# Performance work log

Hardware: AMD Instinct MI355X
Metric: run time of the kernel (lower is better)

## Reference

```python
import jax, jax.numpy as jnp
import numpy as np

N_WINDOWS = 4
WIN_H, WIN_W = 512, 512          # module 'size'
IMG_H, IMG_W = 1024, 1024        # 2x2 tiling of windows
N_MASKS = 32                     # n_windows * masks_per_window
MPW = N_MASKS // N_WINDOWS       # 8 masks per window (channel 0 of each block = background)
SLOT_DIM = 64
SIM_THRESH = 0.1                 # module 'similarity'


def setup_inputs() -> dict:
    key = jax.random.key(0)
    k1, k2 = jax.random.split(key)
    masks = jax.random.normal(k1, (1, N_MASKS, IMG_H, IMG_W), dtype=jnp.float32)
    slot_features = jax.random.normal(k2, (N_WINDOWS, MPW - 1, SLOT_DIM), dtype=jnp.float32)
    # static window layout, equivalent to keys ['w_0_0','w_512_0','w_0_512','w_512_512']
    pad_left = jnp.array([0, WIN_W, 0, WIN_W], dtype=jnp.int32)
    pad_top = jnp.array([0, 0, WIN_H, WIN_H], dtype=jnp.int32)
    return {"masks": masks, "slot_features": slot_features,
            "pad_left": pad_left, "pad_top": pad_top}


def _merge_windows(masks, slot_features, pl, pt):
    """pl, pt: python int lists (static metadata parsed from keys)."""
    B, C, H, W = masks.shape
    mpw = C // N_WINDOWS

    # --- to_one_hot: argmax over channel dim, one-hot back to [B,C,H,W] float ---
    ids = jnp.argmax(masks, axis=1)                                   # [B,H,W]
    m = jnp.moveaxis(jax.nn.one_hot(ids, C, dtype=masks.dtype), -1, 1)  # [B,C,H,W]

    ranges = [(i * mpw, (i + 1) * mpw) for i in range(N_WINDOWS)]

    # --- adjacency over window pads (static) ---
    adjacency = []
    for i in range(N_WINDOWS):
        for j in range(i + 1, N_WINDOWS):
            if pt[i] == pt[j] and abs(pl[i] - pl[j]) == WIN_W:
                adjacency.append((i, j, True) if pl[i] < pl[j] else (j, i, True))
            if pl[i] == pl[j] and abs(pt[i] - pt[j]) == WIN_H:
                adjacency.append((i, j, False) if pt[i] < pt[j] else (j, i, False))

    # --- per-channel edge-touch booleans (vectorized replacement of set building) ---
    edge_l = jnp.zeros((C,), bool)
    edge_r = jnp.zeros((C,), bool)
    edge_t = jnp.zeros((C,), bool)
    edge_b = jnp.zeros((C,), bool)
    for wi, (s, e) in enumerate(ranges):
        ys, ye = max(pt[wi], 0), min(pt[wi] + WIN_H, H)
        xs, xe = max(pl[wi], 0), min(pl[wi] + WIN_W, W)
        if ys >= ye or xs >= xe:
            continue
        win = m[0, s:e, ys:ye, xs:xe]                # [mpw, hh, ww]
        edge_l = edge_l.at[s:e].set(jnp.any(win[:, :, 0] == 1, axis=-1))
        edge_r = edge_r.at[s:e].set(jnp.any(win[:, :, -1] == 1, axis=-1))
        edge_t = edge_t.at[s:e].set(jnp.any(win[:, 0, :] == 1, axis=-1))
        edge_b = edge_b.at[s:e].set(jnp.any(win[:, -1, :] == 1, axis=-1))

    # --- static candidate pair list (background channels ci % mpw == 0 excluded) ---
    ci_l, cj_l, wi_l, wj_l, hz_l = [], [], [], [], []
    for wi, wj, horiz in adjacency:
        si, ei = ranges[wi]
        sj, ej = ranges[wj]
        for ci in range(si + 1, ei):
            for cj in range(sj + 1, ej):
                ci_l.append(ci); cj_l.append(cj)
                wi_l.append(wi); wj_l.append(wj); hz_l.append(horiz)
    P = len(ci_l)
    if P == 0:
        return m

    ci_a = jnp.array(ci_l, jnp.int32)
    cj_a = jnp.array(cj_l, jnp.int32)
    horiz = jnp.array(hz_l)

    # --- cosine similarities for all pairs at once ---
    sf_n = slot_features / (jnp.linalg.norm(slot_features, axis=-1, keepdims=True) + 1e-8)
    rel_i = np.array(ci_l) % mpw - 1
    rel_j = np.array(cj_l) % mpw - 1
    fi = sf_n[np.array(wi_l), rel_i]                 # [P, D]
    fj = sf_n[np.array(wj_l), rel_j]
    sims = jnp.sum(fi * fj, axis=-1)                 # [P]

    edge_ok = jnp.where(horiz, edge_r[ci_a] & edge_l[cj_a], edge_b[ci_a] & edge_t[cj_a])
    passing = edge_ok & (sims > SIM_THRESH)          # [P]

    # --- sequential dedup/merge scan (order-dependent, like the torch loop) ---
    def step(carry, xs):
        m, merged = carry
        ci, cj, ok = xs
        cond = ok & ~merged[ci] & ~merged[cj]
        keep = jnp.minimum(ci, cj)
        rem = jnp.maximum(ci, cj)
        rem_ch = jnp.take(m, rem, axis=1)            # [B,H,W]
        m = m.at[:, keep].add(jnp.where(cond, rem_ch, 0.0))
        m = m.at[:, rem].set(jnp.where(cond, jnp.zeros_like(rem_ch), rem_ch))
        merged = merged.at[rem].set(merged[rem] | cond)
        return (m, merged), None

    (m, _), _ = jax.lax.scan(step, (m, jnp.zeros((C,), bool)), (ci_a, cj_a, passing))
    return m


def reference(masks, slot_features, pad_left, pad_top):
    # pads encode the (static) window layout parsed from the string keys
    pl = [int(v) for v in np.asarray(pad_left)]
    pt = [int(v) for v in np.asarray(pad_top)]
    return _merge_windows(masks, slot_features, pl, pt)
```

## Files before the change

### kernel.cpp

```cpp
#include <hip/hip_runtime.h>

#define IMG_H 1024
#define IMG_W 1024
#define NPIX (IMG_H * IMG_W)
#define N_MASKS 32
#define N_WINDOWS 4
#define MPW 8
#define WIN_H 512
#define WIN_W 512
#define SIM_THRESH 0.1f
#define NBLK 1024

typedef float vf4 __attribute__((ext_vector_type(4)));

#define WS_EDGE  0
#define WS_IDS   (NBLK * 16)

__global__ __launch_bounds__(256) void k_argmax(const float* __restrict__ masks,
                                                const int* __restrict__ pl,
                                                const int* __restrict__ pt,
                                                uint4* __restrict__ edge_blocks,
                                                unsigned char* __restrict__ ids) {
    __shared__ int spl[4], spt[4];
    __shared__ unsigned sem[4];
    const int tid = threadIdx.x;
    if (tid < 4) { spl[tid] = pl[tid]; spt[tid] = pt[tid]; sem[tid] = 0u; }
    __syncthreads();

    const int idx = (blockIdx.x * 256 + tid) * 4;

    float bv0, bv1, bv2, bv3;
    int bc0 = 0, bc1 = 0, bc2 = 0, bc3 = 0;
    {
        const float4 v = *(const float4*)(masks + idx);
        bv0 = v.x; bv1 = v.y; bv2 = v.z; bv3 = v.w;
    }
#pragma unroll
    for (int c = 1; c < N_MASKS; c++) {
        const float4 v = *(const float4*)(masks + (size_t)c * NPIX + idx);
        if (v.x > bv0) { bv0 = v.x; bc0 = c; }
        if (v.y > bv1) { bv1 = v.y; bc1 = c; }
        if (v.z > bv2) { bv2 = v.z; bc2 = c; }
        if (v.w > bv3) { bv3 = v.w; bc3 = c; }
    }
    *(uchar4*)(ids + idx) = make_uchar4((unsigned char)bc0, (unsigned char)bc1,
                                        (unsigned char)bc2, (unsigned char)bc3);

    const int y = idx >> 10;
    const int x0 = idx & (IMG_W - 1);
    const int bcs[4] = {bc0, bc1, bc2, bc3};
#pragma unroll
    for (int wi = 0; wi < N_WINDOWS; wi++) {
        const int xs = max(spl[wi], 0), xe = min(spl[wi] + WIN_W, IMG_W);
        const int ys = max(spt[wi], 0), ye = min(spt[wi] + WIN_H, IMG_H);
        if (ys >= ye || xs >= xe) continue;
        if (y < ys || y >= ye) continue;
#pragma unroll
        for (int k = 0; k < 4; k++) {
            const int x = x0 + k;
            if (x < xs || x >= xe) continue;
            const int c = bcs[k];
            if ((c >> 3) != wi) continue;
            const unsigned bit = 1u << c;
            if (x == xs)     atomicOr(&sem[0], bit);
            if (x == xe - 1) atomicOr(&sem[1], bit);
            if (y == ys)     atomicOr(&sem[2], bit);
            if (y == ye - 1) atomicOr(&sem[3], bit);
        }
    }
    __syncthreads();
    if (tid == 0) edge_blocks[blockIdx.x] = make_uint4(sem[0], sem[1], sem[2], sem[3]);
}

__global__ __launch_bounds__(256) void k_merge_write(const unsigned char* __restrict__ ids,
                                                     const float* __restrict__ sf,
                                                     const int* __restrict__ pl,
                                                     const int* __restrict__ pt,
                                                     const uint4* __restrict__ edge_blocks,
                                                     float* __restrict__ out) {
    __shared__ float sfn[28 * 65];
    __shared__ unsigned step_word[512];
    __shared__ uint4 wred[4];
    __shared__ unsigned fedge[4];
    __shared__ int sP;
    __shared__ int loc[32];

    const int tid = threadIdx.x;
    const int lane = tid & 63;
    const int wave = tid >> 6;

    unsigned el = 0, er = 0, et = 0, eb = 0;
    for (int b = tid; b < NBLK; b += 256) {
        const uint4 w = edge_blocks[b];
        el |= w.x; er |= w.y; et |= w.z; eb |= w.w;
    }
#pragma unroll
    for (int off = 1; off < 64; off <<= 1) {
        el |= __shfl_xor(el, off);
        er |= __shfl_xor(er, off);
        et |= __shfl_xor(et, off);
        eb |= __shfl_xor(eb, off);
    }
    if (lane == 0) wred[wave] = make_uint4(el, er, et, eb);

#pragma unroll
    for (int i = 0; i < 7; i++) {
        const int r = wave + 4 * i;
        const float v = sf[r * 64 + lane];
        float s = v * v;
#pragma unroll
        for (int off = 1; off < 64; off <<= 1) s += __shfl_xor(s, off);
        sfn[r * 65 + lane] = v * (1.0f / (sqrtf(s) + 1e-8f));
    }
    __syncthreads();

    if (tid == 0) {
        unsigned fl = wred[0].x | wred[1].x | wred[2].x | wred[3].x;
        unsigned fr = wred[0].y | wred[1].y | wred[2].y | wred[3].y;
        unsigned ft = wred[0].z | wred[1].z | wred[2].z | wred[3].z;
        unsigned fb = wred[0].w | wred[1].w | wred[2].w | wred[3].w;
        fedge[0] = fl; fedge[1] = fr; fedge[2] = ft; fedge[3] = fb;

        int lpl[4], lpt[4];
        for (int i = 0; i < 4; i++) { lpl[i] = pl[i]; lpt[i] = pt[i]; }
        int aI[8], aJ[8], aH[8], na = 0;
        for (int i = 0; i < N_WINDOWS; i++)
            for (int j = i + 1; j < N_WINDOWS; j++) {
                if (lpt[i] == lpt[j] && abs(lpl[i] - lpl[j]) == WIN_W) {
                    if (lpl[i] < lpl[j]) { aI[na] = i; aJ[na] = j; }
                    else                 { aI[na] = j; aJ[na] = i; }
                    aH[na] = 1; na++;
                }
                if (lpl[i] == lpl[j] && abs(lpt[i] - lpt[j]) == WIN_H) {
                    if (lpt[i] < lpt[j]) { aI[na] = i; aJ[na] = j; }
                    else                 { aI[na] = j; aJ[na] = i; }
                    aH[na] = 0; na++;
                }
            }
        int P = 0;
        for (int a = 0; a < na; a++)
            for (int ci = aI[a] * MPW + 1; ci < (aI[a] + 1) * MPW; ci++)
                for (int cj = aJ[a] * MPW + 1; cj < (aJ[a] + 1) * MPW; cj++)
                    step_word[P++] = (unsigned)ci | ((unsigned)cj << 8)
                                   | ((unsigned)aH[a] << 16);
        sP = P;
    }
    __syncthreads();

    const int P = sP;
    {
        const unsigned ger = fedge[1], gel = fedge[0], geb = fedge[3], get = fedge[2];
        for (int p = tid; p < P; p += 256) {
            const unsigned w = step_word[p];
            const int ci = w & 255, cj = (w >> 8) & 255, hz = (w >> 16) & 1;
            const float* fi = &sfn[((ci >> 3) * (MPW - 1) + (ci & 7) - 1) * 65];
            const float* fj = &sfn[((cj >> 3) * (MPW - 1) + (cj & 7) - 1) * 65];
            float s = 0.f;
#pragma unroll
            for (int k = 0; k < 64; k++) s += fi[k] * fj[k];
            const bool eok = hz ? (((ger >> ci) & 1u) && ((gel >> cj) & 1u))
                                : (((geb >> ci) & 1u) && ((get >> cj) & 1u));
            if (eok && s > SIM_THRESH) step_word[p] = w | (1u << 17);
        }
    }
    __syncthreads();

    if (wave == 0) {
        unsigned merged = 0;
        int myloc = lane;
        for (int p = 0; p < P; p++) {
            const unsigned w = step_word[p];
            if (w >> 17) {
                const int ci = w & 255, cj = (w >> 8) & 255;
                if (!((merged >> ci) & 1u) && !((merged >> cj) & 1u)) {
                    const int keep = min(ci, cj), rem = max(ci, cj);
                    if (myloc == rem) myloc = keep;
                    merged |= 1u << rem;
                }
            }
        }
        if (lane < 32) loc[lane] = myloc;
    }
    __syncthreads();

    const int idx = (blockIdx.x * 256 + tid) * 4;
    const uchar4 id4 = *(const uchar4*)(ids + idx);
    const int r0 = loc[id4.x], r1 = loc[id4.y], r2 = loc[id4.z], r3 = loc[id4.w];
#pragma unroll
    for (int c = 0; c < N_MASKS; c++) {
        vf4 v;
        v.x = (r0 == c) ? 1.0f : 0.0f;
        v.y = (r1 == c) ? 1.0f : 0.0f;
        v.z = (r2 == c) ? 1.0f : 0.0f;
        v.w = (r3 == c) ? 1.0f : 0.0f;
        __builtin_nontemporal_store(v, (vf4*)(out + (size_t)c * NPIX + idx));
    }
}

extern "C" void kernel_launch(void* const* d_in, const int* in_sizes, int n_in,
                              void* d_out, int out_size, void* d_ws, size_t ws_size,
                              hipStream_t stream) {
    const float* masks = (const float*)d_in[0];
    const float* sf    = (const float*)d_in[1];
    const int*   pl    = (const int*)d_in[2];
    const int*   pt    = (const int*)d_in[3];
    float* out = (float*)d_out;

    char* ws = (char*)d_ws;
    uint4* edge_blocks = (uint4*)(ws + WS_EDGE);
    unsigned char* ids = (unsigned char*)(ws + WS_IDS);

    k_argmax<<<NBLK, 256, 0, stream>>>(masks, pl, pt, edge_blocks, ids);
    k_merge_write<<<NBLK, 256, 0, stream>>>(ids, sf, pl, pt, edge_blocks, out);
}
```

Before: 262.2 us.

## Fuse argmax and merge-write into one kernel with inter-block flag sync

Replaces the two kernels with one. Eight blocks recompute argmax only along the window border pixels to build the edge masks, and block 8 builds the merge table from them. All blocks compute their own argmax and spin-wait on a global flag before writing the one-hot output. This removes the per-pixel ids round-trip through memory, the per-block edge atomics and the second launch. In exchange it relies on the low-index blocks being resident, and it never resets the MAGIC flags between calls, so a later call can read stale merge results.

Measured after the change: 578.7 us. +120.7%, slower.

```diff
diff --git a/kernel.cpp b/kernel.cpp
--- a/kernel.cpp
+++ b/kernel.cpp
@@ -10,25 +10,172 @@
 #define WIN_W 512
 #define SIM_THRESH 0.1f
 #define NBLK 1024
+#define MAGIC 0x13579BDFu
 
 typedef float vf4 __attribute__((ext_vector_type(4)));
 
-#define WS_EDGE  0
-#define WS_IDS   (NBLK * 16)
-
-__global__ __launch_bounds__(256) void k_argmax(const float* __restrict__ masks,
-                                                const int* __restrict__ pl,
-                                                const int* __restrict__ pt,
-                                                uint4* __restrict__ edge_blocks,
-                                                unsigned char* __restrict__ ids) {
+
+__global__ __launch_bounds__(256, 4) void k_fused(const float* __restrict__ masks,
+                                                  const float* __restrict__ sf,
+                                                  const int* __restrict__ pl,
+                                                  const int* __restrict__ pt,
+                                                  unsigned* __restrict__ ws,
+                                                  float* __restrict__ out) {
+    unsigned* edges = ws;
+    unsigned* bflag = ws + 32;
+    unsigned* locg  = ws + 48;
+    unsigned* lflag = ws + 80;
+
     __shared__ int spl[4], spt[4];
-    __shared__ unsigned sem[4];
+    __shared__ unsigned segmask[2];
+    __shared__ int sloc[32];
+    __shared__ float sfn[28 * 65];
+    __shared__ unsigned step_word[512];
+    __shared__ unsigned fedge[4];
+    __shared__ int sP;
+
     const int tid = threadIdx.x;
-    if (tid < 4) { spl[tid] = pl[tid]; spt[tid] = pt[tid]; sem[tid] = 0u; }
+    const int lane = tid & 63;
+    const int wave = tid >> 6;
+    const int b = blockIdx.x;
+
+    if (tid < 4) { spl[tid] = pl[tid]; spt[tid] = pt[tid]; }
+    if (tid < 2) segmask[tid] = 0u;
     __syncthreads();
 
-    const int idx = (blockIdx.x * 256 + tid) * 4;
-
+    if (b < 8) {
+        for (int k = 0; k < 2; k++) {
+            const int s = 2 * b + k;
+            const int wi = s >> 2, side = s & 3;
+            const int xs = max(spl[wi], 0), xe = min(spl[wi] + WIN_W, IMG_W);
+            const int ys = max(spt[wi], 0), ye = min(spt[wi] + WIN_H, IMG_H);
+            if (ys >= ye || xs >= xe) continue;
+            const int L = (side < 2) ? (ye - ys) : (xe - xs);
+            for (int u = tid; u < L; u += 256) {
+                int x, y;
+                if      (side == 0) { x = xs;     y = ys + u; }
+                else if (side == 1) { x = xe - 1; y = ys + u; }
+                else if (side == 2) { y = ys;     x = xs + u; }
+                else                { y = ye - 1; x = xs + u; }
+                const int p = y * IMG_W + x;
+                float bv = masks[p];
+                int bc = 0;
+#pragma unroll
+                for (int c = 1; c < N_MASKS; c++) {
+                    const float v = masks[(size_t)c * NPIX + p];
+                    if (v > bv) { bv = v; bc = c; }
+                }
+                if ((bc >> 3) == wi) atomicOr(&segmask[k], 1u << bc);
+            }
+        }
+        __syncthreads();
+        if (tid == 0) {
+            unsigned e[4] = {0u, 0u, 0u, 0u};
+            e[(2 * b) & 3]     |= segmask[0];
+            e[(2 * b + 1) & 3] |= segmask[1];
+#pragma unroll
+            for (int i = 0; i < 4; i++)
+                __hip_atomic_store(&edges[4 * b + i], e[i],
+                                   __ATOMIC_RELAXED, __HIP_MEMORY_SCOPE_AGENT);
+            __hip_atomic_store(&bflag[b], MAGIC,
+                               __ATOMIC_RELEASE, __HIP_MEMORY_SCOPE_AGENT);
+        }
+    } else if (b == 8) {
+        if (tid < 8) {
+            while (__hip_atomic_load(&bflag[tid], __ATOMIC_ACQUIRE,
+                                     __HIP_MEMORY_SCOPE_AGENT) != MAGIC)
+                __builtin_amdgcn_s_sleep(8);
+        }
+        __syncthreads();
+        if (tid == 0) {
+            unsigned e0 = 0, e1 = 0, e2 = 0, e3 = 0;
+            for (int i = 0; i < 8; i++) {
+                e0 |= __hip_atomic_load(&edges[4 * i + 0], __ATOMIC_RELAXED, __HIP_MEMORY_SCOPE_AGENT);
+                e1 |= __hip_atomic_load(&edges[4 * i + 1], __ATOMIC_RELAXED, __HIP_MEMORY_SCOPE_AGENT);
+                e2 |= __hip_atomic_load(&edges[4 * i + 2], __ATOMIC_RELAXED, __HIP_MEMORY_SCOPE_AGENT);
+                e3 |= __hip_atomic_load(&edges[4 * i + 3], __ATOMIC_RELAXED, __HIP_MEMORY_SCOPE_AGENT);
+            }
+            fedge[0] = e0; fedge[1] = e1; fedge[2] = e2; fedge[3] = e3;
+        }
+#pragma unroll
+        for (int i = 0; i < 7; i++) {
+            const int r = wave + 4 * i;
+            const float v = sf[r * 64 + lane];
+            float s2 = v * v;
+#pragma unroll
+            for (int off = 1; off < 64; off <<= 1) s2 += __shfl_xor(s2, off);
+            sfn[r * 65 + lane] = v * (1.0f / (sqrtf(s2) + 1e-8f));
+        }
+        __syncthreads();
+        if (tid == 0) {
+            int lpl[4], lpt[4];
+            for (int i = 0; i < 4; i++) { lpl[i] = spl[i]; lpt[i] = spt[i]; }
+            int aI[8], aJ[8], aH[8], na = 0;
+            for (int i = 0; i < N_WINDOWS; i++)
+                for (int j = i + 1; j < N_WINDOWS; j++) {
+                    if (lpt[i] == lpt[j] && abs(lpl[i] - lpl[j]) == WIN_W) {
+                        if (lpl[i] < lpl[j]) { aI[na] = i; aJ[na] = j; }
+                        else                 { aI[na] = j; aJ[na] = i; }
+                        aH[na] = 1; na++;
+                    }
+                    if (lpl[i] == lpl[j] && abs(lpt[i] - lpt[j]) == WIN_H) {
+                        if (lpt[i] < lpt[j]) { aI[na] = i; aJ[na] = j; }
+                        else                 { aI[na] = j; aJ[na] = i; }
+                        aH[na] = 0; na++;
+                    }
+                }
+            int P = 0;
+            for (int a = 0; a < na; a++)
+                for (int ci = aI[a] * MPW + 1; ci < (aI[a] + 1) * MPW; ci++)
+                    for (int cj = aJ[a] * MPW + 1; cj < (aJ[a] + 1) * MPW; cj++)
+                        step_word[P++] = (unsigned)ci | ((unsigned)cj << 8)
+                                       | ((unsigned)aH[a] << 16);
+            sP = P;
+        }
+        __syncthreads();
+        const int P = sP;
+        {
+            const unsigned gel = fedge[0], ger = fedge[1], get = fedge[2], geb = fedge[3];
+            for (int p = tid; p < P; p += 256) {
+                const unsigned w = step_word[p];
+                const int ci = w & 255, cj = (w >> 8) & 255, hz = (w >> 16) & 1;
+                const float* fi = &sfn[((ci >> 3) * (MPW - 1) + (ci & 7) - 1) * 65];
+                const float* fj = &sfn[((cj >> 3) * (MPW - 1) + (cj & 7) - 1) * 65];
+                float s = 0.f;
+#pragma unroll
+                for (int k2 = 0; k2 < 64; k2++) s += fi[k2] * fj[k2];
+                const bool eok = hz ? (((ger >> ci) & 1u) && ((gel >> cj) & 1u))
+                                    : (((geb >> ci) & 1u) && ((get >> cj) & 1u));
+                if (eok && s > SIM_THRESH) step_word[p] = w | (1u << 17);
+            }
+        }
+        __syncthreads();
+        if (wave == 0) {
+            unsigned merged = 0;
+            int myloc = lane;
+            for (int p = 0; p < P; p++) {
+                const unsigned w = step_word[p];
+                if (w >> 17) {
+                    const int ci = w & 255, cj = (w >> 8) & 255;
+                    if (!((merged >> ci) & 1u) && !((merged >> cj) & 1u)) {
+                        const int keep = min(ci, cj), rem = max(ci, cj);
+                        if (myloc == rem) myloc = keep;
+                        merged |= 1u << rem;
+                    }
+                }
+            }
+            if (lane < 32)
+                __hip_atomic_store(&locg[lane], (unsigned)myloc,
+                                   __ATOMIC_RELAXED, __HIP_MEMORY_SCOPE_AGENT);
+        }
+        __syncthreads();
+        if (tid == 0) {
+            __threadfence();
+            __hip_atomic_store(lflag, MAGIC, __ATOMIC_RELEASE, __HIP_MEMORY_SCOPE_AGENT);
+        }
+    }
+
+    const int idx = (b * 256 + tid) * 4;
     float bv0, bv1, bv2, bv3;
     int bc0 = 0, bc1 = 0, bc2 = 0, bc3 = 0;
     {
@@ -43,149 +190,19 @@
         if (v.z > bv2) { bv2 = v.z; bc2 = c; }
         if (v.w > bv3) { bv3 = v.w; bc3 = c; }
     }
-    *(uchar4*)(ids + idx) = make_uchar4((unsigned char)bc0, (unsigned char)bc1,
-                                        (unsigned char)bc2, (unsigned char)bc3);
-
-    const int y = idx >> 10;
-    const int x0 = idx & (IMG_W - 1);
-    const int bcs[4] = {bc0, bc1, bc2, bc3};
-#pragma unroll
-    for (int wi = 0; wi < N_WINDOWS; wi++) {
-        const int xs = max(spl[wi], 0), xe = min(spl[wi] + WIN_W, IMG_W);
-        const int ys = max(spt[wi], 0), ye = min(spt[wi] + WIN_H, IMG_H);
-        if (ys >= ye || xs >= xe) continue;
-        if (y < ys || y >= ye) continue;
-#pragma unroll
-        for (int k = 0; k < 4; k++) {
-            const int x = x0 + k;
-            if (x < xs || x >= xe) continue;
-            const int c = bcs[k];
-            if ((c >> 3) != wi) continue;
-            const unsigned bit = 1u << c;
-            if (x == xs)     atomicOr(&sem[0], bit);
-            if (x == xe - 1) atomicOr(&sem[1], bit);
-            if (y == ys)     atomicOr(&sem[2], bit);
-            if (y == ye - 1) atomicOr(&sem[3], bit);
-        }
+
+    if (tid == 0) {
+        while (__hip_atomic_load(lflag, __ATOMIC_ACQUIRE,
+                                 __HIP_MEMORY_SCOPE_AGENT) != MAGIC)
+            __builtin_amdgcn_s_sleep(8);
     }
     __syncthreads();
-    if (tid == 0) edge_blocks[blockIdx.x] = make_uint4(sem[0], sem[1], sem[2], sem[3]);
-}
-
-__global__ __launch_bounds__(256) void k_merge_write(const unsigned char* __restrict__ ids,
-                                                     const float* __restrict__ sf,
-                                                     const int* __restrict__ pl,
-                                                     const int* __restrict__ pt,
-                                                     const uint4* __restrict__ edge_blocks,
-                                                     float* __restrict__ out) {
-    __shared__ float sfn[28 * 65];
-    __shared__ unsigned step_word[512];
-    __shared__ uint4 wred[4];
-    __shared__ unsigned fedge[4];
-    __shared__ int sP;
-    __shared__ int loc[32];
-
-    const int tid = threadIdx.x;
-    const int lane = tid & 63;
-    const int wave = tid >> 6;
-
-    unsigned el = 0, er = 0, et = 0, eb = 0;
-    for (int b = tid; b < NBLK; b += 256) {
-        const uint4 w = edge_blocks[b];
-        el |= w.x; er |= w.y; et |= w.z; eb |= w.w;
-    }
-#pragma unroll
-    for (int off = 1; off < 64; off <<= 1) {
-        el |= __shfl_xor(el, off);
-        er |= __shfl_xor(er, off);
-        et |= __shfl_xor(et, off);
-        eb |= __shfl_xor(eb, off);
-    }
-    if (lane == 0) wred[wave] = make_uint4(el, er, et, eb);
-
-#pragma unroll
-    for (int i = 0; i < 7; i++) {
-        const int r = wave + 4 * i;
-        const float v = sf[r * 64 + lane];
-        float s = v * v;
-#pragma unroll
-        for (int off = 1; off < 64; off <<= 1) s += __shfl_xor(s, off);
-        sfn[r * 65 + lane] = v * (1.0f / (sqrtf(s) + 1e-8f));
-    }
+    if (tid < 32)
+        sloc[tid] = (int)__hip_atomic_load(&locg[tid], __ATOMIC_RELAXED,
+                                           __HIP_MEMORY_SCOPE_AGENT);
     __syncthreads();
 
-    if (tid == 0) {
-        unsigned fl = wred[0].x | wred[1].x | wred[2].x | wred[3].x;
-        unsigned fr = wred[0].y | wred[1].y | wred[2].y | wred[3].y;
-        unsigned ft = wred[0].z | wred[1].z | wred[2].z | wred[3].z;
-        unsigned fb = wred[0].w | wred[1].w | wred[2].w | wred[3].w;
-        fedge[0] = fl; fedge[1] = fr; fedge[2] = ft; fedge[3] = fb;
-
-        int lpl[4], lpt[4];
-        for (int i = 0; i < 4; i++) { lpl[i] = pl[i]; lpt[i] = pt[i]; }
-        int aI[8], aJ[8], aH[8], na = 0;
-        for (int i = 0; i < N_WINDOWS; i++)
-            for (int j = i + 1; j < N_WINDOWS; j++) {
-                if (lpt[i] == lpt[j] && abs(lpl[i] - lpl[j]) == WIN_W) {
-                    if (lpl[i] < lpl[j]) { aI[na] = i; aJ[na] = j; }
-                    else                 { aI[na] = j; aJ[na] = i; }
-                    aH[na] = 1; na++;
-                }
-                if (lpl[i] == lpl[j] && abs(lpt[i] - lpt[j]) == WIN_H) {
-                    if (lpt[i] < lpt[j]) { aI[na] = i; aJ[na] = j; }
-                    else                 { aI[na] = j; aJ[na] = i; }
-                    aH[na] = 0; na++;
-                }
-            }
-        int P = 0;
-        for (int a = 0; a < na; a++)
-            for (int ci = aI[a] * MPW + 1; ci < (aI[a] + 1) * MPW; ci++)
-                for (int cj = aJ[a] * MPW + 1; cj < (aJ[a] + 1) * MPW; cj++)
-                    step_word[P++] = (unsigned)ci | ((unsigned)cj << 8)
-                                   | ((unsigned)aH[a] << 16);
-        sP = P;
-    }
-    __syncthreads();
-
-    const int P = sP;
-    {
-        const unsigned ger = fedge[1], gel = fedge[0], geb = fedge[3], get = fedge[2];
-        for (int p = tid; p < P; p += 256) {
-            const unsigned w = step_word[p];
-            const int ci = w & 255, cj = (w >> 8) & 255, hz = (w >> 16) & 1;
-            const float* fi = &sfn[((ci >> 3) * (MPW - 1) + (ci & 7) - 1) * 65];
-            const float* fj = &sfn[((cj >> 3) * (MPW - 1) + (cj & 7) - 1) * 65];
-            float s = 0.f;
-#pragma unroll
-            for (int k = 0; k < 64; k++) s += fi[k] * fj[k];
-            const bool eok = hz ? (((ger >> ci) & 1u) && ((gel >> cj) & 1u))
-                                : (((geb >> ci) & 1u) && ((get >> cj) & 1u));
-            if (eok && s > SIM_THRESH) step_word[p] = w | (1u << 17);
-        }
-    }
-    __syncthreads();
-
-    if (wave == 0) {
-        unsigned merged = 0;
-        int myloc = lane;
-        for (int p = 0; p < P; p++) {
-            const unsigned w = step_word[p];
-            if (w >> 17) {
-                const int ci = w & 255, cj = (w >> 8) & 255;
-                if (!((merged >> ci) & 1u) && !((merged >> cj) & 1u)) {
-                    const int keep = min(ci, cj), rem = max(ci, cj);
-                    if (myloc == rem) myloc = keep;
-                    merged |= 1u << rem;
-                }
-            }
-        }
-        if (lane < 32) loc[lane] = myloc;
-    }
-    __syncthreads();
-
-    const int idx = (blockIdx.x * 256 + tid) * 4;
-    const uchar4 id4 = *(const uchar4*)(ids + idx);
-    const int r0 = loc[id4.x], r1 = loc[id4.y], r2 = loc[id4.z], r3 = loc[id4.w];
+    const int r0 = sloc[bc0], r1 = sloc[bc1], r2 = sloc[bc2], r3 = sloc[bc3];
 #pragma unroll
     for (int c = 0; c < N_MASKS; c++) {
         vf4 v;
@@ -205,11 +222,7 @@
     const int*   pl    = (const int*)d_in[2];
     const int*   pt    = (const int*)d_in[3];
     float* out = (float*)d_out;
-
-    char* ws = (char*)d_ws;
-    uint4* edge_blocks = (uint4*)(ws + WS_EDGE);
-    unsigned char* ids = (unsigned char*)(ws + WS_IDS);
-
-    k_argmax<<<NBLK, 256, 0, stream>>>(masks, pl, pt, edge_blocks, ids);
-    k_merge_write<<<NBLK, 256, 0, stream>>>(ids, sf, pl, pt, edge_blocks, out);
+    unsigned* ws = (unsigned*)d_ws;
+
+    k_fused<<<NBLK, 256, 0, stream>>>(masks, sf, pl, pt, ws, out);
 }
```
